# Kernel tuning notes

Measured on AMD Instinct MI355X. Metric: run time of the kernel, lower is better.

The kernel has to match this reference:

```python
import jax, jax.numpy as jnp
import numpy as np

H, L, D, R = 16, 4096, 64, 128   # heads, seq len, head dim, FAVOR+ feature dim
S_SCALE = 0.125                  # attention inner-product scaling S
CHUNK = 128                      # chunk size for causal linear attention
EPS = 1e-10                      # module's self.epsilon denominator guard


def _get_proj(d, r, seed=0):
    # get_proj(R, D, orthogonal=True, hyperbolic=True): QR-orthogonalized
    # Gaussian block rescaled by chi column norms, then [W, -W].
    rng = np.random.RandomState(seed)
    rh = r // 2
    w = rng.randn(d, rh)
    chis = np.linalg.norm(w, ord=2, axis=0, keepdims=True)
    qm, _ = np.linalg.qr(w, mode='reduced')
    w = qm * chis
    return np.concatenate((w, -w), axis=1).astype(np.float32)  # (D, R)


def setup_inputs() -> dict:
    key = jax.random.key(0)
    kq, kk, kv = jax.random.split(key, 3)
    q = jax.random.normal(kq, (H, L, D), dtype=jnp.float32)
    k = jax.random.normal(kk, (H, L, D), dtype=jnp.float32)
    v = jax.random.normal(kv, (H, L, D), dtype=jnp.float32)
    W = jnp.asarray(_get_proj(D, R))
    return {"T": 64, "k": k, "q": q, "v": v, "W": W}


def _phi(x, W):
    # FAVOR+ feature map: x' = x * S^0.5 / D^0.25;
    # phi(x) = exp(W^T x' - ||x'||^2 / 2) / sqrt(R)
    xs = x * (S_SCALE ** 0.5 / D ** 0.25)            # (H, L, D)
    Wx = jnp.einsum('hld,dr->hlr', xs, W)            # (H, L, R)
    sq = 0.5 * jnp.sum(xs * xs, axis=-1, keepdims=True)
    return jnp.exp(Wx - sq) / (R ** 0.5)             # (H, L, R)


def reference(T, k, q, v, W):
    # Deterministic FAVOR+ estimator of the strictly-causal softmax attention
    # Pred_l = sum_{j<l} v_j exp(S<q_l,k_j>) / sum_{i<l} exp(S<q_l,k_i>)
    # which the tree+sampling machinery approximates (T = sampling budget,
    # irrelevant for the exact kernel estimate). Chunked linear attention.
    del T
    pq = _phi(q, W)                                  # (H, L, R)
    pk = _phi(k, W)                                  # (H, L, R)
    nc = L // CHUNK
    pq_c = pq.reshape(H, nc, CHUNK, R)
    pk_c = pk.reshape(H, nc, CHUNK, R)
    v_c = v.reshape(H, nc, CHUNK, D)
    # per-chunk KV summaries and exclusive prefix over chunks
    skv = jnp.einsum('hncr,hncd->hnrd', pk_c, v_c)   # (H, nc, R, D)
    zk = jnp.sum(pk_c, axis=2)                       # (H, nc, R)
    skv_prev = jnp.cumsum(skv, axis=1) - skv         # exclusive
    zk_prev = jnp.cumsum(zk, axis=1) - zk
    num_inter = jnp.einsum('hncr,hnrd->hncd', pq_c, skv_prev)
    den_inter = jnp.einsum('hncr,hnr->hnc', pq_c, zk_prev)
    # intra-chunk strictly-causal part (j < l)
    A = jnp.einsum('hncr,hnsr->hncs', pq_c, pk_c)    # (H, nc, C, C)
    mask = jnp.tril(jnp.ones((CHUNK, CHUNK), dtype=A.dtype), k=-1)
    A = A * mask
    num_intra = jnp.einsum('hncs,hnsd->hncd', A, v_c)
    den_intra = jnp.sum(A, axis=-1)
    out = (num_inter + num_intra) / (den_inter + den_intra + EPS)[..., None]
    return out.reshape(H, L, D)
```

## Files before the change

kernel.cpp:

```cpp
#include <hip/hip_runtime.h>

#define H 16
#define L 4096
#define D 64
#define R 128
#define CHUNK 128
#define NC 32
#define HL (H * L)
#define HN (H * NC)
#define EPS 1e-10f
#define XS_SCALE 0.125f
#define PHI_SCALE 0.08838834764831845f

typedef __attribute__((ext_vector_type(8))) short bf8;
typedef __attribute__((ext_vector_type(16))) float facc16;

__device__ __forceinline__ unsigned short f2b(float f) {
    unsigned u = __float_as_uint(f);
    return (unsigned short)((u + 0x7fffu + ((u >> 16) & 1u)) >> 16);
}
__device__ __forceinline__ float b2f(unsigned short s) {
    return __uint_as_float(((unsigned)s) << 16);
}

__global__ __launch_bounds__(256) void phi_kernel(const float* __restrict__ q,
                                                  const float* __restrict__ k,
                                                  const float* __restrict__ W,
                                                  unsigned short* __restrict__ pq,
                                                  unsigned short* __restrict__ pk) {
    __shared__ __align__(16) unsigned short Wt[128 * 64];
    __shared__ __align__(16) unsigned short xs[128 * 64];
    __shared__ float sq[128];
    const int tid = threadIdx.x;
    const int isq = blockIdx.x < (HL / 128);
    const float* x = isq ? q : k;
    unsigned short* phi = isq ? pq : pk;
    const size_t row0 = (size_t)(isq ? blockIdx.x : blockIdx.x - HL / 128) * 128;

    for (int i = tid; i < 128 * 64; i += 256) {
        int r = i & 127, d = i >> 7;
        Wt[(unsigned)((r * 64 + d) ^ ((r & 7) << 3))] = f2b(W[d * 128 + r]);
    }
    for (int i = tid; i < 2048; i += 256) {
        int row = i >> 4, d0 = (i & 15) * 4;
        const float4 vv = *(const float4*)(x + (row0 + row) * 64 + d0);
        float a0 = vv.x * XS_SCALE, a1 = vv.y * XS_SCALE;
        float a2 = vv.z * XS_SCALE, a3 = vv.w * XS_SCALE;
        float ss = a0 * a0 + a1 * a1 + a2 * a2 + a3 * a3;
        ss += __shfl_xor(ss, 1); ss += __shfl_xor(ss, 2);
        ss += __shfl_xor(ss, 4); ss += __shfl_xor(ss, 8);
        if ((tid & 15) == 0) sq[row] = 0.5f * ss;
        unsigned idx = (unsigned)((row * 64 + d0) ^ ((row & 7) << 3));
        unsigned* p = (unsigned*)&xs[idx];
        p[0] = (unsigned)f2b(a0) | ((unsigned)f2b(a1) << 16);
        p[1] = (unsigned)f2b(a2) | ((unsigned)f2b(a3) << 16);
    }
    __syncthreads();

    const int lane = tid & 63, wave = tid >> 6;
    const int lo = lane & 31, hi = lane >> 5;
    const int l0 = wave * 32;
    facc16 acc[4];
    #pragma unroll
    for (int t = 0; t < 4; ++t)
        #pragma unroll
        for (int e = 0; e < 16; ++e) acc[t][e] = 0.f;

    #pragma unroll
    for (int s = 0; s < 4; ++s) {
        const bf8 a = *(const bf8*)&xs[(unsigned)(((l0 + lo) * 64 + 16 * s + 8 * hi) ^ ((lo & 7) << 3))];
        #pragma unroll
        for (int t = 0; t < 4; ++t) {
            const bf8 b = *(const bf8*)&Wt[(unsigned)(((t * 32 + lo) * 64 + 16 * s + 8 * hi) ^ ((lo & 7) << 3))];
            acc[t] = __builtin_amdgcn_mfma_f32_32x32x16_bf16(a, b, acc[t], 0, 0, 0);
        }
    }
    #pragma unroll
    for (int t = 0; t < 4; ++t)
        #pragma unroll
        for (int reg = 0; reg < 16; ++reg) {
            int row = l0 + (reg & 3) + 8 * (reg >> 2) + 4 * hi;
            int col = t * 32 + lo;
            float val = __expf(acc[t][reg] - sq[row]) * PHI_SCALE;
            phi[(row0 + row) * 128 + col] = f2b(val);
        }
}

__global__ __launch_bounds__(256) void skv_kernel(const unsigned short* __restrict__ pk,
                                                  const float* __restrict__ v,
                                                  unsigned short* __restrict__ vT,
                                                  float* __restrict__ skvT,
                                                  float* __restrict__ zk) {
    __shared__ __align__(16) unsigned short pkT[128 * 128];
    __shared__ __align__(16) unsigned short vTl[64 * 128];
    const int tid = threadIdx.x, hn = blockIdx.x;
    const unsigned short* pkg = pk + (size_t)hn * CHUNK * R;
    const float* vg = v + (size_t)hn * CHUNK * D;

    for (int i = tid; i < 2048; i += 256) {
        int c = i & 127, r0 = (i >> 7) * 8;
        bf8 t8 = *(const bf8*)(pkg + c * 128 + r0);
        #pragma unroll
        for (int e = 0; e < 8; ++e)
            pkT[(unsigned)(((r0 + e) * 128 + c) ^ (((r0 + e) & 7) << 3))] = (unsigned short)t8[e];
    }
    for (int i = tid; i < 8192; i += 256) {
        int d = i & 63, c = i >> 6;
        vTl[(unsigned)((d * 128 + c) ^ ((d & 7) << 3))] = f2b(vg[c * 64 + d]);
    }
    __syncthreads();

    unsigned short* vTg = vT + (size_t)hn * D * CHUNK;
    for (int i = tid; i < 1024; i += 256) {
        int d = i >> 4, c0 = (i & 15) * 8;
        *(bf8*)(vTg + d * 128 + c0) = *(const bf8*)&vTl[(unsigned)((d * 128 + c0) ^ ((d & 7) << 3))];
    }
    if (tid < 128) {
        float s = 0.f;
        #pragma unroll
        for (int j = 0; j < 16; ++j) {
            bf8 a8 = *(const bf8*)&pkT[(unsigned)((tid * 128 + 8 * j) ^ ((tid & 7) << 3))];
            #pragma unroll
            for (int e = 0; e < 8; ++e) s += b2f((unsigned short)a8[e]);
        }
        zk[(size_t)hn * 128 + tid] = s;
    }

    const int lane = tid & 63, wave = tid >> 6, lo = lane & 31, hi = lane >> 5;
    facc16 acc[2];
    #pragma unroll
    for (int t = 0; t < 2; ++t)
        #pragma unroll
        for (int e = 0; e < 16; ++e) acc[t][e] = 0.f;
    #pragma unroll
    for (int s = 0; s < 8; ++s) {
        const bf8 b = *(const bf8*)&pkT[(unsigned)(((wave * 32 + lo) * 128 + 16 * s + 8 * hi) ^ ((lo & 7) << 3))];
        #pragma unroll
        for (int db = 0; db < 2; ++db) {
            const bf8 a = *(const bf8*)&vTl[(unsigned)(((db * 32 + lo) * 128 + 16 * s + 8 * hi) ^ ((lo & 7) << 3))];
            acc[db] = __builtin_amdgcn_mfma_f32_32x32x16_bf16(a, b, acc[db], 0, 0, 0);
        }
    }
    float* sg = skvT + (size_t)hn * D * R;
    #pragma unroll
    for (int db = 0; db < 2; ++db)
        #pragma unroll
        for (int reg = 0; reg < 16; ++reg) {
            int row = db * 32 + (reg & 3) + 8 * (reg >> 2) + 4 * hi;
            sg[row * 128 + wave * 32 + lo] = acc[db][reg];
        }
}

__global__ __launch_bounds__(256) void scan_kernel(const float* __restrict__ skvT,
                                                   unsigned short* __restrict__ skvTp,
                                                   const float* __restrict__ zk,
                                                   unsigned short* __restrict__ zkp) {
    const int bid = blockIdx.x;
    if (bid < 512) {
        int id = bid * 256 + threadIdx.x;
        int h = id >> 13, dr = id & 8191;
        const float* p = skvT + (size_t)h * NC * 8192 + dr;
        unsigned short* o = skvTp + (size_t)h * NC * 8192 + dr;
        float run = 0.f;
        #pragma unroll
        for (int n = 0; n < NC; ++n) {
            float t = p[(size_t)n * 8192];
            o[(size_t)n * 8192] = f2b(run);
            run += t;
        }
    } else {
        int id = (bid - 512) * 256 + threadIdx.x;
        int h = id >> 7, r = id & 127;
        const float* p = zk + (size_t)h * NC * 128 + r;
        unsigned short* o = zkp + (size_t)h * NC * 128 + r;
        float run = 0.f;
        #pragma unroll
        for (int n = 0; n < NC; ++n) {
            float t = p[n * 128];
            o[n * 128] = f2b(run);
            run += t;
        }
    }
}

__global__ __launch_bounds__(256) void out_kernel(const unsigned short* __restrict__ pq,
                                                  const unsigned short* __restrict__ pk,
                                                  const unsigned short* __restrict__ vT,
                                                  const unsigned short* __restrict__ skvTp,
                                                  const unsigned short* __restrict__ zkp,
                                                  float* __restrict__ out) {
    __shared__ __align__(16) unsigned short pkl[128 * 128];
    __shared__ __align__(16) unsigned short vTl[64 * 128];
    __shared__ __align__(16) unsigned short svl[64 * 128];
    __shared__ __align__(16) unsigned short dB1[32 * 128];
    __shared__ __align__(16) unsigned short dB2[32 * 128];
    const int tid = threadIdx.x, hn = blockIdx.x;
    const int lane = tid & 63, wave = tid >> 6, lo = lane & 31, hi = lane >> 5;
    const int l0 = wave * 32;

    bf8 qf[8];
    const unsigned short* pqg = pq + (size_t)hn * CHUNK * R;
    #pragma unroll
    for (int s = 0; s < 8; ++s)
        qf[s] = *(const bf8*)(pqg + (l0 + lo) * 128 + 16 * s + 8 * hi);

    const unsigned short* pkg = pk + (size_t)hn * CHUNK * R;
    for (int i = tid; i < 2048; i += 256) {
        int c = i >> 4, rb = (i & 15) * 8;
        *(bf8*)&pkl[(unsigned)((c * 128 + rb) ^ ((c & 7) << 3))] = *(const bf8*)(pkg + c * 128 + rb);
    }
    const unsigned short* vTg = vT + (size_t)hn * D * CHUNK;
    const unsigned short* svg = skvTp + (size_t)hn * D * R;
    for (int i = tid; i < 1024; i += 256) {
        int d = i >> 4, c0 = (i & 15) * 8;
        unsigned idx = (unsigned)((d * 128 + c0) ^ ((d & 7) << 3));
        *(bf8*)&vTl[idx] = *(const bf8*)(vTg + d * 128 + c0);
        *(bf8*)&svl[idx] = *(const bf8*)(svg + d * 128 + c0);
    }
    if (tid < 128) {
        dB1[tid] = 0x3F80;
        dB2[tid] = zkp[(size_t)hn * 128 + tid];
    }
    __syncthreads();

    facc16 acc1[4];
    #pragma unroll
    for (int t = 0; t < 4; ++t)
        #pragma unroll
        for (int e = 0; e < 16; ++e) acc1[t][e] = 0.f;
    #pragma unroll
    for (int s = 0; s < 8; ++s)
        #pragma unroll
        for (int t = 0; t < 4; ++t) {
            const bf8 b = *(const bf8*)&pkl[(unsigned)(((t * 32 + lo) * 128 + 16 * s + 8 * hi) ^ ((lo & 7) << 3))];
            acc1[t] = __builtin_amdgcn_mfma_f32_32x32x16_bf16(qf[s], b, acc1[t], 0, 0, 0);
        }
    __syncthreads();

    #pragma unroll
    for (int t = 0; t < 4; ++t)
        #pragma unroll
        for (int reg = 0; reg < 16; ++reg) {
            int row = l0 + (reg & 3) + 8 * (reg >> 2) + 4 * hi;
            int sc = t * 32 + lo;
            pkl[(unsigned)((row * 128 + sc) ^ ((row & 7) << 3))] = f2b(sc < row ? acc1[t][reg] : 0.f);
        }
    __syncthreads();

    facc16 acc2[3];
    #pragma unroll
    for (int t = 0; t < 3; ++t)
        #pragma unroll
        for (int e = 0; e < 16; ++e) acc2[t][e] = 0.f;
    #pragma unroll
    for (int s = 0; s < 8; ++s) {
        const bf8 a = *(const bf8*)&pkl[(unsigned)(((l0 + lo) * 128 + 16 * s + 8 * hi) ^ ((lo & 7) << 3))];
        #pragma unroll
        for (int t = 0; t < 2; ++t) {
            const bf8 b = *(const bf8*)&vTl[(unsigned)(((t * 32 + lo) * 128 + 16 * s + 8 * hi) ^ ((lo & 7) << 3))];
            acc2[t] = __builtin_amdgcn_mfma_f32_32x32x16_bf16(a, b, acc2[t], 0, 0, 0);
        }
        const bf8 bd = *(const bf8*)&dB1[(unsigned)((lo * 128 + 16 * s + 8 * hi) ^ ((lo & 7) << 3))];
        acc2[2] = __builtin_amdgcn_mfma_f32_32x32x16_bf16(a, bd, acc2[2], 0, 0, 0);
    }
    #pragma unroll
    for (int s = 0; s < 8; ++s) {
        #pragma unroll
        for (int t = 0; t < 2; ++t) {
            const bf8 b = *(const bf8*)&svl[(unsigned)(((t * 32 + lo) * 128 + 16 * s + 8 * hi) ^ ((lo & 7) << 3))];
            acc2[t] = __builtin_amdgcn_mfma_f32_32x32x16_bf16(qf[s], b, acc2[t], 0, 0, 0);
        }
        const bf8 bd = *(const bf8*)&dB2[(unsigned)((lo * 128 + 16 * s + 8 * hi) ^ ((lo & 7) << 3))];
        acc2[2] = __builtin_amdgcn_mfma_f32_32x32x16_bf16(qf[s], bd, acc2[2], 0, 0, 0);
    }

    float* og = out + (size_t)hn * CHUNK * D;
    #pragma unroll
    for (int reg = 0; reg < 16; ++reg) {
        int row = l0 + (reg & 3) + 8 * (reg >> 2) + 4 * hi;
        float dv = __shfl(acc2[2][reg], lane & 32);
        float inv = 1.0f / (dv + EPS);
        og[row * 64 + lo]      = acc2[0][reg] * inv;
        og[row * 64 + 32 + lo] = acc2[1][reg] * inv;
    }
}

extern "C" void kernel_launch(void* const* d_in, const int* in_sizes, int n_in,
                              void* d_out, int out_size, void* d_ws, size_t ws_size,
                              hipStream_t stream) {
    const float* k = (const float*)d_in[1];
    const float* q = (const float*)d_in[2];
    const float* v = (const float*)d_in[3];
    const float* W = (const float*)d_in[4];

    unsigned short* pq = (unsigned short*)d_ws;
    unsigned short* pk = pq + (size_t)HL * R;
    unsigned short* vT = pk + (size_t)HL * R;
    unsigned short* skvTp = vT + (size_t)HN * D * CHUNK;
    float* zk = (float*)(skvTp + (size_t)HN * D * R);
    unsigned short* zkp = (unsigned short*)(zk + (size_t)HN * R);
    float* skvT = (float*)d_out;

    phi_kernel<<<2 * (HL / 128), 256, 0, stream>>>(q, k, W, pq, pk);
    skv_kernel<<<HN, 256, 0, stream>>>(pk, v, vT, skvT, zk);
    scan_kernel<<<520, 256, 0, stream>>>(skvT, skvTp, zk, zkp);
    out_kernel<<<HN, 256, 0, stream>>>(pq, pk, vT, skvTp, zkp, (float*)d_out);
}
```

Baseline: 60.21 us.

## Fuse all stages into one cooperative kernel with grid syncs and LDS reuse

Replaces the four-kernel pipeline (phi, skv, scan, out) with a single cooperative kernel. One block per (head, chunk) computes phi(q) and phi(k) straight into LDS, keeps phi(q) fragments in registers, builds the KV summary, and uses grid-wide syncs around the chunk prefix scan before computing outputs. This avoids writing and re-reading the bf16 pq/pk/vT intermediates through global memory and cuts launch overhead. In exchange it adds two grid barriers and needs 512 blocks co-resident at two per CU, with a three-kernel fallback when the cooperative launch is not possible.

```diff
diff --git a/kernel.cpp b/kernel.cpp
--- a/kernel.cpp
+++ b/kernel.cpp
@@ -1,4 +1,7 @@
 #include <hip/hip_runtime.h>
+#include <hip/hip_cooperative_groups.h>
+
+namespace cg = cooperative_groups;
 
 #define H 16
 #define L 4096
@@ -13,6 +16,7 @@
 #define PHI_SCALE 0.08838834764831845f
 
 typedef __attribute__((ext_vector_type(8))) short bf8;
+typedef __attribute__((ext_vector_type(4))) short bf4;
 typedef __attribute__((ext_vector_type(16))) float facc16;
 
 __device__ __forceinline__ unsigned short f2b(float f) {
@@ -23,27 +27,29 @@
     return __uint_as_float(((unsigned)s) << 16);
 }
 
-__global__ __launch_bounds__(256) void phi_kernel(const float* __restrict__ q,
-                                                  const float* __restrict__ k,
-                                                  const float* __restrict__ W,
-                                                  unsigned short* __restrict__ pq,
-                                                  unsigned short* __restrict__ pk) {
-    __shared__ __align__(16) unsigned short Wt[128 * 64];
-    __shared__ __align__(16) unsigned short xs[128 * 64];
-    __shared__ float sq[128];
-    const int tid = threadIdx.x;
-    const int isq = blockIdx.x < (HL / 128);
-    const float* x = isq ? q : k;
-    unsigned short* phi = isq ? pq : pk;
-    const size_t row0 = (size_t)(isq ? blockIdx.x : blockIdx.x - HL / 128) * 128;
-
-    for (int i = tid; i < 128 * 64; i += 256) {
+template<bool DUMP>
+__device__ __forceinline__ void phase1(
+    const float* __restrict__ q, const float* __restrict__ k,
+    const float* __restrict__ v, const float* __restrict__ W,
+    unsigned short* bufA, unsigned short* bufB, unsigned short* bufC,
+    float* __restrict__ stage, float* __restrict__ zk,
+    unsigned short* __restrict__ pqd, unsigned short* __restrict__ pkd,
+    unsigned short* __restrict__ vTd, bf8* qf, int hn, int tid)
+{
+    unsigned short* Wt = bufC;
+    unsigned short* xs = bufC + 8192;
+    float* sq = (float*)bufB;
+    const int lane = tid & 63, wave = tid >> 6, lo = lane & 31, hi = lane >> 5;
+    const int l0 = wave * 32;
+    const size_t cbase = (size_t)hn * CHUNK * D;
+
+    for (int i = tid; i < 8192; i += 256) {
         int r = i & 127, d = i >> 7;
         Wt[(unsigned)((r * 64 + d) ^ ((r & 7) << 3))] = f2b(W[d * 128 + r]);
     }
     for (int i = tid; i < 2048; i += 256) {
         int row = i >> 4, d0 = (i & 15) * 4;
-        const float4 vv = *(const float4*)(x + (row0 + row) * 64 + d0);
+        float4 vv = *(const float4*)(q + cbase + row * 64 + d0);
         float a0 = vv.x * XS_SCALE, a1 = vv.y * XS_SCALE;
         float a2 = vv.z * XS_SCALE, a3 = vv.w * XS_SCALE;
         float ss = a0 * a0 + a1 * a1 + a2 * a2 + a3 * a3;
@@ -57,171 +63,207 @@
     }
     __syncthreads();
 
-    const int lane = tid & 63, wave = tid >> 6;
-    const int lo = lane & 31, hi = lane >> 5;
-    const int l0 = wave * 32;
-    facc16 acc[4];
+    {
+        facc16 acc[4];
+        #pragma unroll
+        for (int t = 0; t < 4; ++t)
+            #pragma unroll
+            for (int e = 0; e < 16; ++e) acc[t][e] = 0.f;
+        #pragma unroll
+        for (int s = 0; s < 4; ++s) {
+            const bf8 a = *(const bf8*)&xs[(unsigned)(((l0 + lo) * 64 + 16 * s + 8 * hi) ^ ((lo & 7) << 3))];
+            #pragma unroll
+            for (int t = 0; t < 4; ++t) {
+                const bf8 b = *(const bf8*)&Wt[(unsigned)(((t * 32 + lo) * 64 + 16 * s + 8 * hi) ^ ((lo & 7) << 3))];
+                acc[t] = __builtin_amdgcn_mfma_f32_32x32x16_bf16(a, b, acc[t], 0, 0, 0);
+            }
+        }
+        #pragma unroll
+        for (int t = 0; t < 4; ++t)
+            #pragma unroll
+            for (int reg = 0; reg < 16; ++reg) {
+                int row = l0 + (reg & 3) + 8 * (reg >> 2) + 4 * hi;
+                int col = t * 32 + lo;
+                bufA[(unsigned)((row * 128 + col) ^ ((row & 7) << 3))] =
+                    f2b(__expf(acc[t][reg] - sq[row]) * PHI_SCALE);
+            }
+    }
+    __syncthreads();
+
+    #pragma unroll
+    for (int s = 0; s < 8; ++s)
+        qf[s] = *(const bf8*)&bufA[(unsigned)(((l0 + lo) * 128 + 16 * s + 8 * hi) ^ ((lo & 7) << 3))];
+    if constexpr (DUMP) {
+        unsigned short* pg = pqd + (size_t)hn * CHUNK * R;
+        for (int i = tid; i < 2048; i += 256) {
+            int c = i >> 4, rb = (i & 15) * 8;
+            *(bf8*)(pg + c * 128 + rb) = *(const bf8*)&bufA[(unsigned)((c * 128 + rb) ^ ((c & 7) << 3))];
+        }
+    }
+
+    for (int i = tid; i < 2048; i += 256) {
+        int row = i >> 4, d0 = (i & 15) * 4;
+        float4 vv = *(const float4*)(k + cbase + row * 64 + d0);
+        float a0 = vv.x * XS_SCALE, a1 = vv.y * XS_SCALE;
+        float a2 = vv.z * XS_SCALE, a3 = vv.w * XS_SCALE;
+        float ss = a0 * a0 + a1 * a1 + a2 * a2 + a3 * a3;
+        ss += __shfl_xor(ss, 1); ss += __shfl_xor(ss, 2);
+        ss += __shfl_xor(ss, 4); ss += __shfl_xor(ss, 8);
+        if ((tid & 15) == 0) sq[row] = 0.5f * ss;
+        unsigned idx = (unsigned)((row * 64 + d0) ^ ((row & 7) << 3));
+        unsigned* p = (unsigned*)&xs[idx];
+        p[0] = (unsigned)f2b(a0) | ((unsigned)f2b(a1) << 16);
+        p[1] = (unsigned)f2b(a2) | ((unsigned)f2b(a3) << 16);
+    }
+    __syncthreads();
+
+    facc16 acck[4];
     #pragma unroll
     for (int t = 0; t < 4; ++t)
         #pragma unroll
-        for (int e = 0; e < 16; ++e) acc[t][e] = 0.f;
-
+        for (int e = 0; e < 16; ++e) acck[t][e] = 0.f;
     #pragma unroll
     for (int s = 0; s < 4; ++s) {
         const bf8 a = *(const bf8*)&xs[(unsigned)(((l0 + lo) * 64 + 16 * s + 8 * hi) ^ ((lo & 7) << 3))];
         #pragma unroll
         for (int t = 0; t < 4; ++t) {
             const bf8 b = *(const bf8*)&Wt[(unsigned)(((t * 32 + lo) * 64 + 16 * s + 8 * hi) ^ ((lo & 7) << 3))];
-            acc[t] = __builtin_amdgcn_mfma_f32_32x32x16_bf16(a, b, acc[t], 0, 0, 0);
-        }
-    }
-    #pragma unroll
-    for (int t = 0; t < 4; ++t)
-        #pragma unroll
-        for (int reg = 0; reg < 16; ++reg) {
-            int row = l0 + (reg & 3) + 8 * (reg >> 2) + 4 * hi;
-            int col = t * 32 + lo;
-            float val = __expf(acc[t][reg] - sq[row]) * PHI_SCALE;
-            phi[(row0 + row) * 128 + col] = f2b(val);
-        }
-}
-
-__global__ __launch_bounds__(256) void skv_kernel(const unsigned short* __restrict__ pk,
-                                                  const float* __restrict__ v,
-                                                  unsigned short* __restrict__ vT,
-                                                  float* __restrict__ skvT,
-                                                  float* __restrict__ zk) {
-    __shared__ __align__(16) unsigned short pkT[128 * 128];
-    __shared__ __align__(16) unsigned short vTl[64 * 128];
-    const int tid = threadIdx.x, hn = blockIdx.x;
-    const unsigned short* pkg = pk + (size_t)hn * CHUNK * R;
-    const float* vg = v + (size_t)hn * CHUNK * D;
-
-    for (int i = tid; i < 2048; i += 256) {
-        int c = i & 127, r0 = (i >> 7) * 8;
-        bf8 t8 = *(const bf8*)(pkg + c * 128 + r0);
-        #pragma unroll
-        for (int e = 0; e < 8; ++e)
-            pkT[(unsigned)(((r0 + e) * 128 + c) ^ (((r0 + e) & 7) << 3))] = (unsigned short)t8[e];
-    }
+            acck[t] = __builtin_amdgcn_mfma_f32_32x32x16_bf16(a, b, acck[t], 0, 0, 0);
+        }
+    }
+    __syncthreads();
+
+    #pragma unroll
+    for (int t = 0; t < 4; ++t) {
+        int colr = t * 32 + lo;
+        #pragma unroll
+        for (int g = 0; g < 4; ++g) {
+            int c0 = l0 + 8 * g + 4 * hi;
+            bf4 pk4;
+            #pragma unroll
+            for (int e = 0; e < 4; ++e) {
+                unsigned short b = f2b(__expf(acck[t][4 * g + e] - sq[c0 + e]) * PHI_SCALE);
+                pk4[e] = (short)b;
+                bufA[(unsigned)(((c0 + e) * 128 + colr) ^ (((c0 + e) & 7) << 3))] = b;
+            }
+            *(bf4*)&bufC[(unsigned)((colr * 128 + c0) ^ ((colr & 7) << 3))] = pk4;
+        }
+    }
+    __syncthreads();
+
     for (int i = tid; i < 8192; i += 256) {
         int d = i & 63, c = i >> 6;
-        vTl[(unsigned)((d * 128 + c) ^ ((d & 7) << 3))] = f2b(vg[c * 64 + d]);
-    }
-    __syncthreads();
-
-    unsigned short* vTg = vT + (size_t)hn * D * CHUNK;
-    for (int i = tid; i < 1024; i += 256) {
-        int d = i >> 4, c0 = (i & 15) * 8;
-        *(bf8*)(vTg + d * 128 + c0) = *(const bf8*)&vTl[(unsigned)((d * 128 + c0) ^ ((d & 7) << 3))];
+        bufB[(unsigned)((d * 128 + c) ^ ((d & 7) << 3))] = f2b(v[cbase + c * 64 + d]);
     }
     if (tid < 128) {
         float s = 0.f;
         #pragma unroll
         for (int j = 0; j < 16; ++j) {
-            bf8 a8 = *(const bf8*)&pkT[(unsigned)((tid * 128 + 8 * j) ^ ((tid & 7) << 3))];
+            bf8 a8 = *(const bf8*)&bufC[(unsigned)((tid * 128 + 8 * j) ^ ((tid & 7) << 3))];
             #pragma unroll
             for (int e = 0; e < 8; ++e) s += b2f((unsigned short)a8[e]);
         }
         zk[(size_t)hn * 128 + tid] = s;
     }
-
-    const int lane = tid & 63, wave = tid >> 6, lo = lane & 31, hi = lane >> 5;
-    facc16 acc[2];
-    #pragma unroll
-    for (int t = 0; t < 2; ++t)
-        #pragma unroll
-        for (int e = 0; e < 16; ++e) acc[t][e] = 0.f;
-    #pragma unroll
-    for (int s = 0; s < 8; ++s) {
-        const bf8 b = *(const bf8*)&pkT[(unsigned)(((wave * 32 + lo) * 128 + 16 * s + 8 * hi) ^ ((lo & 7) << 3))];
-        #pragma unroll
-        for (int db = 0; db < 2; ++db) {
-            const bf8 a = *(const bf8*)&vTl[(unsigned)(((db * 32 + lo) * 128 + 16 * s + 8 * hi) ^ ((lo & 7) << 3))];
-            acc[db] = __builtin_amdgcn_mfma_f32_32x32x16_bf16(a, b, acc[db], 0, 0, 0);
-        }
-    }
-    float* sg = skvT + (size_t)hn * D * R;
-    #pragma unroll
-    for (int db = 0; db < 2; ++db)
-        #pragma unroll
-        for (int reg = 0; reg < 16; ++reg) {
-            int row = db * 32 + (reg & 3) + 8 * (reg >> 2) + 4 * hi;
-            sg[row * 128 + wave * 32 + lo] = acc[db][reg];
-        }
-}
-
-__global__ __launch_bounds__(256) void scan_kernel(const float* __restrict__ skvT,
-                                                   unsigned short* __restrict__ skvTp,
-                                                   const float* __restrict__ zk,
-                                                   unsigned short* __restrict__ zkp) {
-    const int bid = blockIdx.x;
-    if (bid < 512) {
-        int id = bid * 256 + threadIdx.x;
-        int h = id >> 13, dr = id & 8191;
-        const float* p = skvT + (size_t)h * NC * 8192 + dr;
-        unsigned short* o = skvTp + (size_t)h * NC * 8192 + dr;
-        float run = 0.f;
+    if constexpr (DUMP) {
+        unsigned short* pg = pkd + (size_t)hn * CHUNK * R;
+        for (int i = tid; i < 2048; i += 256) {
+            int c = i >> 4, rb = (i & 15) * 8;
+            *(bf8*)(pg + c * 128 + rb) = *(const bf8*)&bufA[(unsigned)((c * 128 + rb) ^ ((c & 7) << 3))];
+        }
+    }
+    __syncthreads();
+
+    if constexpr (DUMP) {
+        unsigned short* vg2 = vTd + (size_t)hn * D * CHUNK;
+        for (int i = tid; i < 1024; i += 256) {
+            int d = i >> 4, c0 = (i & 15) * 8;
+            *(bf8*)(vg2 + d * 128 + c0) = *(const bf8*)&bufB[(unsigned)((d * 128 + c0) ^ ((d & 7) << 3))];
+        }
+    }
+    {
+        facc16 accs[2];
+        #pragma unroll
+        for (int t = 0; t < 2; ++t)
+            #pragma unroll
+            for (int e = 0; e < 16; ++e) accs[t][e] = 0.f;
+        #pragma unroll
+        for (int s = 0; s < 8; ++s) {
+            const bf8 b = *(const bf8*)&bufC[(unsigned)(((wave * 32 + lo) * 128 + 16 * s + 8 * hi) ^ ((lo & 7) << 3))];
+            #pragma unroll
+            for (int db = 0; db < 2; ++db) {
+                const bf8 a = *(const bf8*)&bufB[(unsigned)(((db * 32 + lo) * 128 + 16 * s + 8 * hi) ^ ((lo & 7) << 3))];
+                accs[db] = __builtin_amdgcn_mfma_f32_32x32x16_bf16(a, b, accs[db], 0, 0, 0);
+            }
+        }
+        float* sg = stage + (size_t)hn * D * R;
+        #pragma unroll
+        for (int db = 0; db < 2; ++db)
+            #pragma unroll
+            for (int reg = 0; reg < 16; ++reg) {
+                int row = db * 32 + (reg & 3) + 8 * (reg >> 2) + 4 * hi;
+                sg[row * 128 + wave * 32 + lo] = accs[db][reg];
+            }
+    }
+}
+
+__device__ __forceinline__ void phase2(const float* __restrict__ stage,
+                                       unsigned short* __restrict__ skvTp,
+                                       const float* __restrict__ zk,
+                                       unsigned short* __restrict__ zkp,
+                                       int bid, int tid)
+{
+    int g = bid * 256 + tid;
+    int h2 = g >> 13, dr = g & 8191;
+    const float* p = stage + (size_t)h2 * NC * 8192 + dr;
+    unsigned short* o = skvTp + (size_t)h2 * NC * 8192 + dr;
+    float run = 0.f;
+    #pragma unroll
+    for (int n = 0; n < NC; ++n) {
+        float t = p[(size_t)n * 8192];
+        o[(size_t)n * 8192] = f2b(run);
+        run += t;
+    }
+    if (g < 2048) {
+        int h3 = g >> 7, r = g & 127;
+        const float* pz = zk + (size_t)h3 * NC * 128 + r;
+        unsigned short* oz = zkp + (size_t)h3 * NC * 128 + r;
+        float runz = 0.f;
         #pragma unroll
         for (int n = 0; n < NC; ++n) {
-            float t = p[(size_t)n * 8192];
-            o[(size_t)n * 8192] = f2b(run);
-            run += t;
-        }
-    } else {
-        int id = (bid - 512) * 256 + threadIdx.x;
-        int h = id >> 7, r = id & 127;
-        const float* p = zk + (size_t)h * NC * 128 + r;
-        unsigned short* o = zkp + (size_t)h * NC * 128 + r;
-        float run = 0.f;
-        #pragma unroll
-        for (int n = 0; n < NC; ++n) {
-            float t = p[n * 128];
-            o[n * 128] = f2b(run);
-            run += t;
-        }
-    }
-}
-
-__global__ __launch_bounds__(256) void out_kernel(const unsigned short* __restrict__ pq,
-                                                  const unsigned short* __restrict__ pk,
-                                                  const unsigned short* __restrict__ vT,
-                                                  const unsigned short* __restrict__ skvTp,
-                                                  const unsigned short* __restrict__ zkp,
-                                                  float* __restrict__ out) {
-    __shared__ __align__(16) unsigned short pkl[128 * 128];
-    __shared__ __align__(16) unsigned short vTl[64 * 128];
-    __shared__ __align__(16) unsigned short svl[64 * 128];
-    __shared__ __align__(16) unsigned short dB1[32 * 128];
-    __shared__ __align__(16) unsigned short dB2[32 * 128];
-    const int tid = threadIdx.x, hn = blockIdx.x;
+            float t2 = pz[n * 128];
+            oz[n * 128] = f2b(runz);
+            runz += t2;
+        }
+    }
+}
+
+__device__ __forceinline__ void phase3(
+    unsigned short* bufA, unsigned short* bufB, unsigned short* bufC,
+    const unsigned short* __restrict__ skvTp, const unsigned short* __restrict__ zkp,
+    const bf8* qf, int hn, int tid, float* __restrict__ out)
+{
     const int lane = tid & 63, wave = tid >> 6, lo = lane & 31, hi = lane >> 5;
     const int l0 = wave * 32;
-
-    bf8 qf[8];
-    const unsigned short* pqg = pq + (size_t)hn * CHUNK * R;
-    #pragma unroll
-    for (int s = 0; s < 8; ++s)
-        qf[s] = *(const bf8*)(pqg + (l0 + lo) * 128 + 16 * s + 8 * hi);
-
-    const unsigned short* pkg = pk + (size_t)hn * CHUNK * R;
-    for (int i = tid; i < 2048; i += 256) {
-        int c = i >> 4, rb = (i & 15) * 8;
-        *(bf8*)&pkl[(unsigned)((c * 128 + rb) ^ ((c & 7) << 3))] = *(const bf8*)(pkg + c * 128 + rb);
-    }
-    const unsigned short* vTg = vT + (size_t)hn * D * CHUNK;
+    __syncthreads();
+
     const unsigned short* svg = skvTp + (size_t)hn * D * R;
     for (int i = tid; i < 1024; i += 256) {
-        int d = i >> 4, c0 = (i & 15) * 8;
-        unsigned idx = (unsigned)((d * 128 + c0) ^ ((d & 7) << 3));
-        *(bf8*)&vTl[idx] = *(const bf8*)(vTg + d * 128 + c0);
-        *(bf8*)&svl[idx] = *(const bf8*)(svg + d * 128 + c0);
-    }
-    if (tid < 128) {
-        dB1[tid] = 0x3F80;
-        dB2[tid] = zkp[(size_t)hn * 128 + tid];
-    }
-    __syncthreads();
+        int d = i >> 4, r0 = (i & 15) * 8;
+        *(bf8*)&bufC[(unsigned)((d * 128 + r0) ^ ((d & 7) << 3))] = *(const bf8*)(svg + d * 128 + r0);
+    }
+    bf8 zf[8], onesf;
+    #pragma unroll
+    for (int e = 0; e < 8; ++e) onesf[e] = (lo == 0) ? (short)0x3F80 : (short)0;
+    #pragma unroll
+    for (int s = 0; s < 8; ++s)
+        #pragma unroll
+        for (int e = 0; e < 8; ++e) zf[s][e] = 0;
+    if (lo == 0) {
+        #pragma unroll
+        for (int s = 0; s < 8; ++s)
+            zf[s] = *(const bf8*)(zkp + (size_t)hn * 128 + 16 * s + 8 * hi);
+    }
 
     facc16 acc1[4];
     #pragma unroll
@@ -232,7 +274,7 @@
     for (int s = 0; s < 8; ++s)
         #pragma unroll
         for (int t = 0; t < 4; ++t) {
-            const bf8 b = *(const bf8*)&pkl[(unsigned)(((t * 32 + lo) * 128 + 16 * s + 8 * hi) ^ ((lo & 7) << 3))];
+            const bf8 b = *(const bf8*)&bufA[(unsigned)(((t * 32 + lo) * 128 + 16 * s + 8 * hi) ^ ((lo & 7) << 3))];
             acc1[t] = __builtin_amdgcn_mfma_f32_32x32x16_bf16(qf[s], b, acc1[t], 0, 0, 0);
         }
     __syncthreads();
@@ -243,7 +285,7 @@
         for (int reg = 0; reg < 16; ++reg) {
             int row = l0 + (reg & 3) + 8 * (reg >> 2) + 4 * hi;
             int sc = t * 32 + lo;
-            pkl[(unsigned)((row * 128 + sc) ^ ((row & 7) << 3))] = f2b(sc < row ? acc1[t][reg] : 0.f);
+            bufA[(unsigned)((row * 128 + sc) ^ ((row & 7) << 3))] = f2b(sc < row ? acc1[t][reg] : 0.f);
         }
     __syncthreads();
 
@@ -254,24 +296,22 @@
         for (int e = 0; e < 16; ++e) acc2[t][e] = 0.f;
     #pragma unroll
     for (int s = 0; s < 8; ++s) {
-        const bf8 a = *(const bf8*)&pkl[(unsigned)(((l0 + lo) * 128 + 16 * s + 8 * hi) ^ ((lo & 7) << 3))];
+        const bf8 a = *(const bf8*)&bufA[(unsigned)(((l0 + lo) * 128 + 16 * s + 8 * hi) ^ ((lo & 7) << 3))];
         #pragma unroll
         for (int t = 0; t < 2; ++t) {
-            const bf8 b = *(const bf8*)&vTl[(unsigned)(((t * 32 + lo) * 128 + 16 * s + 8 * hi) ^ ((lo & 7) << 3))];
+            const bf8 b = *(const bf8*)&bufB[(unsigned)(((t * 32 + lo) * 128 + 16 * s + 8 * hi) ^ ((lo & 7) << 3))];
             acc2[t] = __builtin_amdgcn_mfma_f32_32x32x16_bf16(a, b, acc2[t], 0, 0, 0);
         }
-        const bf8 bd = *(const bf8*)&dB1[(unsigned)((lo * 128 + 16 * s + 8 * hi) ^ ((lo & 7) << 3))];
-        acc2[2] = __builtin_amdgcn_mfma_f32_32x32x16_bf16(a, bd, acc2[2], 0, 0, 0);
+        acc2[2] = __builtin_amdgcn_mfma_f32_32x32x16_bf16(a, onesf, acc2[2], 0, 0, 0);
     }
     #pragma unroll
     for (int s = 0; s < 8; ++s) {
         #pragma unroll
         for (int t = 0; t < 2; ++t) {
-            const bf8 b = *(const bf8*)&svl[(unsigned)(((t * 32 + lo) * 128 + 16 * s + 8 * hi) ^ ((lo & 7) << 3))];
+            const bf8 b = *(const bf8*)&bufC[(unsigned)(((t * 32 + lo) * 128 + 16 * s + 8 * hi) ^ ((lo & 7) << 3))];
             acc2[t] = __builtin_amdgcn_mfma_f32_32x32x16_bf16(qf[s], b, acc2[t], 0, 0, 0);
         }
-        const bf8 bd = *(const bf8*)&dB2[(unsigned)((lo * 128 + 16 * s + 8 * hi) ^ ((lo & 7) << 3))];
-        acc2[2] = __builtin_amdgcn_mfma_f32_32x32x16_bf16(qf[s], bd, acc2[2], 0, 0, 0);
+        acc2[2] = __builtin_amdgcn_mfma_f32_32x32x16_bf16(qf[s], zf[s], acc2[2], 0, 0, 0);
     }
 
     float* og = out + (size_t)hn * CHUNK * D;
@@ -283,6 +323,82 @@
         og[row * 64 + lo]      = acc2[0][reg] * inv;
         og[row * 64 + 32 + lo] = acc2[1][reg] * inv;
     }
+}
+
+__global__ __launch_bounds__(256, 2) void fused_coop(
+    const float* __restrict__ q, const float* __restrict__ k,
+    const float* __restrict__ v, const float* __restrict__ W,
+    unsigned short* __restrict__ skvTp, unsigned short* __restrict__ zkp,
+    float* __restrict__ zk, float* __restrict__ out)
+{
+    __shared__ __align__(16) unsigned short LDSm[40960];
+    unsigned short* bufA = LDSm;
+    unsigned short* bufB = LDSm + 16384;
+    unsigned short* bufC = LDSm + 24576;
+    const int tid = threadIdx.x, hn = blockIdx.x;
+    bf8 qf[8];
+    phase1<false>(q, k, v, W, bufA, bufB, bufC, out, zk,
+                  nullptr, nullptr, nullptr, qf, hn, tid);
+    __threadfence();
+    cg::this_grid().sync();
+    phase2(out, skvTp, zk, zkp, hn, tid);
+    __threadfence();
+    cg::this_grid().sync();
+    __threadfence();
+    phase3(bufA, bufB, bufC, skvTp, zkp, qf, hn, tid, out);
+}
+
+__global__ __launch_bounds__(256, 2) void kA(
+    const float* __restrict__ q, const float* __restrict__ k,
+    const float* __restrict__ v, const float* __restrict__ W,
+    float* __restrict__ stage, float* __restrict__ zk,
+    unsigned short* __restrict__ pqd, unsigned short* __restrict__ pkd,
+    unsigned short* __restrict__ vTd)
+{
+    __shared__ __align__(16) unsigned short LDSm[40960];
+    bf8 qf[8];
+    phase1<true>(q, k, v, W, LDSm, LDSm + 16384, LDSm + 24576, stage, zk,
+                 pqd, pkd, vTd, qf, blockIdx.x, threadIdx.x);
+}
+
+__global__ __launch_bounds__(256) void kB(const float* __restrict__ stage,
+                                          unsigned short* __restrict__ skvTp,
+                                          const float* __restrict__ zk,
+                                          unsigned short* __restrict__ zkp)
+{
+    phase2(stage, skvTp, zk, zkp, blockIdx.x, threadIdx.x);
+}
+
+__global__ __launch_bounds__(256, 2) void kC(
+    const unsigned short* __restrict__ pq, const unsigned short* __restrict__ pk,
+    const unsigned short* __restrict__ vT, const unsigned short* __restrict__ skvTp,
+    const unsigned short* __restrict__ zkp, float* __restrict__ out)
+{
+    __shared__ __align__(16) unsigned short LDSm[32768];
+    unsigned short* bufA = LDSm;
+    unsigned short* bufB = LDSm + 16384;
+    unsigned short* bufC = LDSm + 24576;
+    const int tid = threadIdx.x, hn = blockIdx.x;
+    const int lane = tid & 63, wave = tid >> 6, lo = lane & 31, hi = lane >> 5;
+    const int l0 = wave * 32;
+
+    bf8 qf[8];
+    const unsigned short* pqg = pq + (size_t)hn * CHUNK * R;
+    #pragma unroll
+    for (int s = 0; s < 8; ++s)
+        qf[s] = *(const bf8*)(pqg + (l0 + lo) * 128 + 16 * s + 8 * hi);
+
+    const unsigned short* pkg = pk + (size_t)hn * CHUNK * R;
+    for (int i = tid; i < 2048; i += 256) {
+        int c = i >> 4, rb = (i & 15) * 8;
+        *(bf8*)&bufA[(unsigned)((c * 128 + rb) ^ ((c & 7) << 3))] = *(const bf8*)(pkg + c * 128 + rb);
+    }
+    const unsigned short* vTg = vT + (size_t)hn * D * CHUNK;
+    for (int i = tid; i < 1024; i += 256) {
+        int d = i >> 4, c0 = (i & 15) * 8;
+        *(bf8*)&bufB[(unsigned)((d * 128 + c0) ^ ((d & 7) << 3))] = *(const bf8*)(vTg + d * 128 + c0);
+    }
+    phase3(bufA, bufB, bufC, skvTp, zkp, qf, hn, tid, out);
 }
 
 extern "C" void kernel_launch(void* const* d_in, const int* in_sizes, int n_in,
@@ -292,17 +408,30 @@
     const float* q = (const float*)d_in[2];
     const float* v = (const float*)d_in[3];
     const float* W = (const float*)d_in[4];
-
-    unsigned short* pq = (unsigned short*)d_ws;
+    float* out = (float*)d_out;
+
+    unsigned short* skvTp = (unsigned short*)d_ws;
+    unsigned short* zkp = skvTp + (size_t)HN * D * R;
+    float* zk = (float*)(zkp + (size_t)HN * R);
+    unsigned short* pq = (unsigned short*)(zk + (size_t)HN * R);
     unsigned short* pk = pq + (size_t)HL * R;
     unsigned short* vT = pk + (size_t)HL * R;
-    unsigned short* skvTp = vT + (size_t)HN * D * CHUNK;
-    float* zk = (float*)(skvTp + (size_t)HN * D * R);
-    unsigned short* zkp = (unsigned short*)(zk + (size_t)HN * R);
-    float* skvT = (float*)d_out;
-
-    phi_kernel<<<2 * (HL / 128), 256, 0, stream>>>(q, k, W, pq, pk);
-    skv_kernel<<<HN, 256, 0, stream>>>(pk, v, vT, skvT, zk);
-    scan_kernel<<<520, 256, 0, stream>>>(skvT, skvTp, zk, zkp);
-    out_kernel<<<HN, 256, 0, stream>>>(pq, pk, vT, skvTp, zkp, (float*)d_out);
-}
+
+    int nb = 0;
+    hipError_t qrc = hipOccupancyMaxActiveBlocksPerMultiprocessor(
+        &nb, (const void*)fused_coop, 256, 0);
+    bool launched = false;
+    if (qrc == hipSuccess && nb >= 2) {
+        void* kargs[8] = {(void*)&q, (void*)&k, (void*)&v, (void*)&W,
+                          (void*)&skvTp, (void*)&zkp, (void*)&zk, (void*)&out};
+        hipError_t rc = hipLaunchCooperativeKernel((const void*)fused_coop,
+                                                   dim3(HN), dim3(256), kargs, 0, stream);
+        launched = (rc == hipSuccess);
+        if (!launched) (void)hipGetLastError();
+    }
+    if (!launched) {
+        kA<<<HN, 256, 0, stream>>>(q, k, v, W, out, zk, pq, pk, vT);
+        kB<<<HN, 256, 0, stream>>>(out, skvTp, zk, zkp);
+        kC<<<HN, 256, 0, stream>>>(pq, pk, vT, skvTp, zkp, out);
+    }
+}
```

After: 54.90 us. 8.8% less time.
